# Kernel tuning notes

Hardware: AMD Instinct MI355X
Metric: run time of the kernel (lower is better)

## Reference

```python
import jax, jax.numpy as jnp
import numpy as np

B, T, I, H, R, O = 128, 512, 64, 512, 4, 64
NOISE_STD = 0.05
TAU = 0.2


def setup_inputs() -> dict:
    key = jax.random.key(0)
    ks = jax.random.split(key, 16)
    s = 0.08  # xavier-ish scale to keep gates in sane range
    return {
        "u": jax.random.normal(ks[0], (B, T, I), jnp.float32),
        "x0": jnp.zeros((B, H), jnp.float32),
        "noise": jax.random.normal(ks[1], (T, B, H), jnp.float32),
        "W_ir": jax.random.normal(ks[2], (H, I), jnp.float32) * s,
        "b_ir": jax.random.normal(ks[3], (H,), jnp.float32) * s,
        "W_iz": jax.random.normal(ks[4], (H, I), jnp.float32) * s,
        "b_iz": jax.random.normal(ks[5], (H,), jnp.float32) * s,
        "W_ih": jax.random.normal(ks[6], (H, I), jnp.float32) * s,
        "b_ih": jax.random.normal(ks[7], (H,), jnp.float32) * s,
        "N_hr": jax.random.normal(ks[8], (H, R), jnp.float32) * s,
        "M_hr": jax.random.normal(ks[9], (H, R), jnp.float32) * s,
        "N_hz": jax.random.normal(ks[10], (H, R), jnp.float32) * s,
        "M_hz": jax.random.normal(ks[11], (H, R), jnp.float32) * s,
        "N_hh": jax.random.normal(ks[12], (H, R), jnp.float32) * s,
        "M_hh": jax.random.normal(ks[13], (H, R), jnp.float32) * s,
        "W_out": jax.random.normal(ks[14], (O, H), jnp.float32) * s,
        "b_out": jax.random.normal(ks[15], (O,), jnp.float32) * s,
    }


def reference(u, x0, noise, W_ir, b_ir, W_iz, b_iz, W_ih, b_ih,
              N_hr, M_hr, N_hz, M_hz, N_hh, M_hh, W_out, b_out):
    scale = 1.0 / u.shape[-1] * 0 + 1.0 / N_hr.shape[0]  # 1/H (cont mode)
    scale = 1.0 / N_hr.shape[0]
    u_t = jnp.transpose(u, (1, 0, 2))  # [T,B,I]
    # precompute input projections for all steps (same math as per-step Linear)
    ir = jnp.einsum('tbi,hi->tbh', u_t, W_ir) + b_ir
    iz = jnp.einsum('tbi,hi->tbh', u_t, W_iz) + b_iz
    ih = jnp.einsum('tbi,hi->tbh', u_t, W_ih) + b_ih

    def step(x, inp):
        ir_t, iz_t, ih_t, n_t = inp
        hr = (x @ N_hr) @ M_hr.T * scale
        hz = (x @ N_hz) @ M_hz.T * scale
        r = jax.nn.sigmoid(ir_t + hr)
        z = jax.nn.sigmoid(iz_t + hz)
        hh = ((r * x) @ N_hh) @ M_hh.T * scale
        g = jnp.tanh(ih_t + hh)
        rec_x = (1.0 - z) * g + z * x
        x_new = x + NOISE_STD * n_t + TAU * (-x + rec_x)  # cont mode
        return x_new, x_new

    x_last, traj = jax.lax.scan(step, x0, (ir, iz, ih, noise))  # traj: [T,B,H]
    traj = jnp.transpose(traj, (1, 0, 2))  # [B,T,H]
    output = jnp.einsum('bth,oh->bto', traj, W_out) + b_out
    return output, x_last, traj
```

## Files before the change

kernel.cpp:

```cpp
#include <hip/hip_runtime.h>
#include <hip/hip_bf16.h>
#include <stdint.h>

#define Bv 128
#define Tv 512
#define Iv 64
#define Hv 512
#define Ov 64

typedef __attribute__((ext_vector_type(8))) short bv8;
typedef __attribute__((ext_vector_type(4))) float fv4;
typedef __attribute__((ext_vector_type(4))) unsigned uv4;
typedef __attribute__((ext_vector_type(2))) unsigned uv2;
typedef __attribute__((ext_vector_type(8))) unsigned short usv8;

static __device__ __forceinline__ unsigned short f2bf(float f) {
  unsigned u = __builtin_bit_cast(unsigned, f);
  u += 0x7fffu + ((u >> 16) & 1u);
  return (unsigned short)(u >> 16);
}
static __device__ __forceinline__ float bf2f(unsigned short s) {
  return __builtin_bit_cast(float, ((unsigned)s) << 16);
}
static __device__ __forceinline__ float sgm(float a) {
  return __builtin_amdgcn_rcpf(1.0f + __expf(-a));
}

template <int CTRL>
static __device__ __forceinline__ float dpp_add(float v) {
  int t = __builtin_amdgcn_update_dpp(0, __builtin_bit_cast(int, v), CTRL, 0xF, 0xF, true);
  return v + __builtin_bit_cast(float, t);
}

static __device__ __forceinline__ float wave_red(float v) {
  v = dpp_add<0xB1>(v);
  v = dpp_add<0x4E>(v);
  v = dpp_add<0x124>(v);
  v = dpp_add<0x128>(v);
  unsigned a = __builtin_bit_cast(unsigned, v);
  uv2 p = __builtin_amdgcn_permlane16_swap(a, a, false, false);
  v = __builtin_bit_cast(float, p[0]) + __builtin_bit_cast(float, p[1]);
  a = __builtin_bit_cast(unsigned, v);
  uv2 q = __builtin_amdgcn_permlane32_swap(a, a, false, false);
  v = __builtin_bit_cast(float, q[0]) + __builtin_bit_cast(float, q[1]);
  return v;
}

__global__ __launch_bounds__(256) void proj_kernel(
    const float* __restrict__ u,
    const float* __restrict__ Wir, const float* __restrict__ bir,
    const float* __restrict__ Wiz, const float* __restrict__ biz,
    const float* __restrict__ Wih, const float* __restrict__ bih,
    unsigned* __restrict__ irz, unsigned short* __restrict__ ihb)
{
  __shared__ __align__(16) unsigned short As[64][72];
  const int bt0 = blockIdx.x * 64;
  const int h0b = blockIdx.y * 64;
  const int tid = threadIdx.x;
  {
    const int r = tid >> 2, ksg = (tid & 3) * 16;
    const float* src = u + (size_t)(bt0 + r) * Iv + ksg;
    unsigned short tmp[16];
#pragma unroll
    for (int i = 0; i < 16; i += 4) {
      float4 v = *(const float4*)(src + i);
      tmp[i] = f2bf(v.x); tmp[i+1] = f2bf(v.y); tmp[i+2] = f2bf(v.z); tmp[i+3] = f2bf(v.w);
    }
    *(uv4*)&As[r][ksg]     = *(uv4*)&tmp[0];
    *(uv4*)&As[r][ksg + 8] = *(uv4*)&tmp[8];
  }
  __syncthreads();
  const int wave = tid >> 6, lane = tid & 63;
  const int n = lane & 15, q = lane >> 4;
  const int h = h0b + wave * 16 + n;
  const float* Wg[3] = {Wir, Wiz, Wih};
  bv8 bfrag[3][2];
#pragma unroll
  for (int g = 0; g < 3; ++g)
#pragma unroll
    for (int ks = 0; ks < 2; ++ks) {
      const float* wp = Wg[g] + (size_t)h * Iv + ks * 32 + q * 8;
      float4 w0 = *(const float4*)wp, w1 = *(const float4*)(wp + 4);
      bv8 f;
      f[0] = (short)f2bf(w0.x); f[1] = (short)f2bf(w0.y);
      f[2] = (short)f2bf(w0.z); f[3] = (short)f2bf(w0.w);
      f[4] = (short)f2bf(w1.x); f[5] = (short)f2bf(w1.y);
      f[6] = (short)f2bf(w1.z); f[7] = (short)f2bf(w1.w);
      bfrag[g][ks] = f;
    }
  const float bs0 = bir[h], bs1 = biz[h], bs2 = bih[h];
#pragma unroll
  for (int sub = 0; sub < 4; ++sub) {
    bv8 a0 = *(const bv8*)&As[sub * 16 + n][q * 8];
    bv8 a1 = *(const bv8*)&As[sub * 16 + n][32 + q * 8];
    fv4 ar = {0.f,0.f,0.f,0.f}, az = {0.f,0.f,0.f,0.f}, ah = {0.f,0.f,0.f,0.f};
    ar = __builtin_amdgcn_mfma_f32_16x16x32_bf16(a0, bfrag[0][0], ar, 0, 0, 0);
    ar = __builtin_amdgcn_mfma_f32_16x16x32_bf16(a1, bfrag[0][1], ar, 0, 0, 0);
    az = __builtin_amdgcn_mfma_f32_16x16x32_bf16(a0, bfrag[1][0], az, 0, 0, 0);
    az = __builtin_amdgcn_mfma_f32_16x16x32_bf16(a1, bfrag[1][1], az, 0, 0, 0);
    ah = __builtin_amdgcn_mfma_f32_16x16x32_bf16(a0, bfrag[2][0], ah, 0, 0, 0);
    ah = __builtin_amdgcn_mfma_f32_16x16x32_bf16(a1, bfrag[2][1], ah, 0, 0, 0);
#pragma unroll
    for (int j = 0; j < 4; ++j) {
      const int row = bt0 + sub * 16 + q * 4 + j;
      const size_t slot = (size_t)row * Hv + h;
      irz[slot] = ((unsigned)f2bf(az[j] + bs1) << 16) | (unsigned)f2bf(ar[j] + bs0);
      ihb[slot] = f2bf(ah[j] + bs2);
    }
  }
}

struct Buf { uv4 irz0, irz1; usv8 ih; fv4 nz0, nz1; };
#define IRZ(bf, j) ((j) < 4 ? (bf).irz0[(j)] : (bf).irz1[(j) - 4])
#define NZE(bf, j) ((j) < 4 ? (bf).nz0[(j)]  : (bf).nz1[(j) - 4])

__global__ __launch_bounds__(64, 1) void scan_kernel(
    const float* __restrict__ x0, const float* __restrict__ noise,
    const float* __restrict__ Nhr, const float* __restrict__ Mhr,
    const float* __restrict__ Nhz, const float* __restrict__ Mhz,
    const float* __restrict__ Nhh, const float* __restrict__ Mhh,
    unsigned* __restrict__ traj, const unsigned short* __restrict__ ihb,
    float* __restrict__ xlast)
{
  const int b = blockIdx.x, lane = threadIdx.x;
  const int h0 = lane * 8;
  fv4 nr[8], nz_[8], nh[8], mr[8], mz[8], mh[8];
#pragma unroll
  for (int j = 0; j < 8; ++j) {
    nr[j]  = *(const fv4*)(Nhr + (size_t)(h0 + j) * 4);
    nz_[j] = *(const fv4*)(Nhz + (size_t)(h0 + j) * 4);
    nh[j]  = *(const fv4*)(Nhh + (size_t)(h0 + j) * 4);
    mr[j]  = *(const fv4*)(Mhr + (size_t)(h0 + j) * 4);
    mz[j]  = *(const fv4*)(Mhz + (size_t)(h0 + j) * 4);
    mh[j]  = *(const fv4*)(Mhh + (size_t)(h0 + j) * 4);
  }
#pragma unroll
  for (int j = 0; j < 8; ++j) {
    asm("" : "+v"(nr[j]), "+v"(nz_[j]), "+v"(nh[j]));
    asm("" : "+v"(mr[j]), "+v"(mz[j]), "+v"(mh[j]));
  }
  float x[8];
  {
    fv4 a = *(const fv4*)(x0 + (size_t)b * Hv + h0);
    fv4 c = *(const fv4*)(x0 + (size_t)b * Hv + h0 + 4);
#pragma unroll
    for (int j = 0; j < 4; ++j) { x[j] = a[j]; x[j + 4] = c[j]; }
  }
  const size_t rowbase = (size_t)b * Tv * Hv + h0;
  const size_t nbase = (size_t)b * Hv + h0;
  Buf A, Bb;
  auto LOAD = [&](Buf& bf, int t) {
    const unsigned* p = traj + rowbase + (size_t)t * Hv;
    bf.irz0 = *(const uv4*)p;
    bf.irz1 = *(const uv4*)(p + 4);
    bf.ih = *(const usv8*)(ihb + rowbase + (size_t)t * Hv);
    const float* np = noise + (size_t)t * (Bv * Hv) + nbase;
    bf.nz0 = *(const fv4*)np;
    bf.nz1 = *(const fv4*)(np + 4);
  };
  const float sc = 1.0f / 512.0f;
  auto STEP = [&](const Buf& bf, int t) {
    float sr[4] = {0, 0, 0, 0}, sz[4] = {0, 0, 0, 0};
#pragma unroll
    for (int j = 0; j < 8; ++j)
#pragma unroll
      for (int r = 0; r < 4; ++r) {
        sr[r] = fmaf(x[j], nr[j][r], sr[r]);
        sz[r] = fmaf(x[j], nz_[j][r], sz[r]);
      }
#pragma unroll
    for (int r = 0; r < 4; ++r) {
      sr[r] = wave_red(sr[r]) * sc;
      sz[r] = wave_red(sz[r]) * sc;
    }
    float rr[8], zz[8];
#pragma unroll
    for (int j = 0; j < 8; ++j) {
      float hr = fmaf(sr[3], mr[j][3], fmaf(sr[2], mr[j][2], fmaf(sr[1], mr[j][1], sr[0] * mr[j][0])));
      float hz = fmaf(sz[3], mz[j][3], fmaf(sz[2], mz[j][2], fmaf(sz[1], mz[j][1], sz[0] * mz[j][0])));
      unsigned w = IRZ(bf, j);
      rr[j] = sgm(bf2f((unsigned short)(w & 0xffffu)) + hr);
      zz[j] = sgm(bf2f((unsigned short)(w >> 16)) + hz);
    }
    float sh[4] = {0, 0, 0, 0};
#pragma unroll
    for (int j = 0; j < 8; ++j) {
      float rx = rr[j] * x[j];
#pragma unroll
      for (int r = 0; r < 4; ++r) sh[r] = fmaf(rx, nh[j][r], sh[r]);
    }
#pragma unroll
    for (int r = 0; r < 4; ++r) sh[r] = wave_red(sh[r]) * sc;
#pragma unroll
    for (int j = 0; j < 8; ++j) {
      float hh = fmaf(sh[3], mh[j][3], fmaf(sh[2], mh[j][2], fmaf(sh[1], mh[j][1], sh[0] * mh[j][0])));
      float a = bf2f(bf.ih[j]) + hh;
      a = fminf(fmaxf(a, -15.f), 15.f);
      float e = __expf(-2.f * a);
      float g = (1.f - e) * __builtin_amdgcn_rcpf(1.f + e);
      x[j] = x[j] + 0.05f * NZE(bf, j) + 0.2f * (1.f - zz[j]) * (g - x[j]);
    }
    float* op = (float*)(traj + rowbase + (size_t)t * Hv);
    fv4 s0 = {x[0], x[1], x[2], x[3]}, s1 = {x[4], x[5], x[6], x[7]};
    *(fv4*)op = s0;
    *(fv4*)(op + 4) = s1;
  };
  LOAD(A, 0);
  for (int t = 0; t < Tv; t += 2) {
    LOAD(Bb, t + 1);
    STEP(A, t);
    if (t + 2 < Tv) LOAD(A, t + 2);
    STEP(Bb, t + 1);
  }
  {
    fv4 s0 = {x[0], x[1], x[2], x[3]}, s1 = {x[4], x[5], x[6], x[7]};
    *(fv4*)(xlast + nbase) = s0;
    *(fv4*)(xlast + nbase + 4) = s1;
  }
}

__global__ __launch_bounds__(256) void outproj_kernel(
    const float* __restrict__ traj, const float* __restrict__ Wout,
    const float* __restrict__ bout, float* __restrict__ out)
{
  __shared__ __align__(16) unsigned short As[64][40];
  const int bt0 = blockIdx.x * 64;
  const int tid = threadIdx.x;
  const int wave = tid >> 6, lane = tid & 63;
  const int n = lane & 15, q = lane >> 4;
  const int o = wave * 16 + n;
  const float bo = bout[o];
  fv4 acc[4] = {{0.f,0.f,0.f,0.f},{0.f,0.f,0.f,0.f},{0.f,0.f,0.f,0.f},{0.f,0.f,0.f,0.f}};
  const int r = tid >> 2, ksg = (tid & 3) * 8;
  for (int ks = 0; ks < 16; ++ks) {
    __syncthreads();
    {
      const float* src = traj + (size_t)(bt0 + r) * Hv + ks * 32 + ksg;
      float4 v0 = *(const float4*)src, v1 = *(const float4*)(src + 4);
      unsigned short tmp[8];
      tmp[0] = f2bf(v0.x); tmp[1] = f2bf(v0.y); tmp[2] = f2bf(v0.z); tmp[3] = f2bf(v0.w);
      tmp[4] = f2bf(v1.x); tmp[5] = f2bf(v1.y); tmp[6] = f2bf(v1.z); tmp[7] = f2bf(v1.w);
      *(uv4*)&As[r][ksg] = *(uv4*)&tmp[0];
    }
    __syncthreads();
    const float* wp = Wout + (size_t)o * Hv + ks * 32 + q * 8;
    float4 w0 = *(const float4*)wp, w1 = *(const float4*)(wp + 4);
    bv8 bf;
    bf[0] = (short)f2bf(w0.x); bf[1] = (short)f2bf(w0.y);
    bf[2] = (short)f2bf(w0.z); bf[3] = (short)f2bf(w0.w);
    bf[4] = (short)f2bf(w1.x); bf[5] = (short)f2bf(w1.y);
    bf[6] = (short)f2bf(w1.z); bf[7] = (short)f2bf(w1.w);
#pragma unroll
    for (int sub = 0; sub < 4; ++sub) {
      bv8 af = *(const bv8*)&As[sub * 16 + n][q * 8];
      acc[sub] = __builtin_amdgcn_mfma_f32_16x16x32_bf16(af, bf, acc[sub], 0, 0, 0);
    }
  }
#pragma unroll
  for (int sub = 0; sub < 4; ++sub)
#pragma unroll
    for (int j = 0; j < 4; ++j) {
      const int row = bt0 + sub * 16 + q * 4 + j;
      out[(size_t)row * Ov + o] = acc[sub][j] + bo;
    }
}

extern "C" void kernel_launch(void* const* d_in, const int* in_sizes, int n_in,
                              void* d_out, int out_size, void* d_ws, size_t ws_size,
                              hipStream_t stream) {
  const float* u    = (const float*)d_in[0];
  const float* x0   = (const float*)d_in[1];
  const float* noise= (const float*)d_in[2];
  const float* Wir  = (const float*)d_in[3];
  const float* bir  = (const float*)d_in[4];
  const float* Wiz  = (const float*)d_in[5];
  const float* biz  = (const float*)d_in[6];
  const float* Wih  = (const float*)d_in[7];
  const float* bih  = (const float*)d_in[8];
  const float* Nhr  = (const float*)d_in[9];
  const float* Mhr  = (const float*)d_in[10];
  const float* Nhz  = (const float*)d_in[11];
  const float* Mhz  = (const float*)d_in[12];
  const float* Nhh  = (const float*)d_in[13];
  const float* Mhh  = (const float*)d_in[14];
  const float* Wout = (const float*)d_in[15];
  const float* bout = (const float*)d_in[16];

  float* out   = (float*)d_out;
  float* xlast = out + (size_t)Bv * Tv * Ov;
  float* traj  = xlast + (size_t)Bv * Hv;
  unsigned short* ihbuf = (unsigned short*)d_ws;

  proj_kernel<<<dim3(1024, 8, 1), 256, 0, stream>>>(
      u, Wir, bir, Wiz, biz, Wih, bih, (unsigned*)traj, ihbuf);
  scan_kernel<<<dim3(128, 1, 1), 64, 0, stream>>>(
      x0, noise, Nhr, Mhr, Nhz, Mhz, Nhh, Mhh, (unsigned*)traj, ihbuf, xlast);
  outproj_kernel<<<dim3(1024, 1, 1), 256, 0, stream>>>(traj, Wout, bout, out);
}
```

Before: 762.4 us.

## Split each batch row's hidden dim across two waves with LDS partial-sum exchange

The scan kernel now assigns each batch element to two waves, each owning 256 hidden units at 4 per lane, and packs 4 batch elements into a 512-thread block instead of one wave per block. The two rank-4 reductions per step are combined across the wave pair through shared memory behind block-wide __syncthreads, and the 1/H scale is folded into the M matrices at load time. The aim is to halve the serial per-lane work and the size of each per-step load on the latency-bound recurrence. In exchange it adds two block barriers per timestep that also tie together the four unrelated batch elements in the block.

Result: slower. 915.7 us (+20.1%).

```diff
diff --git a/kernel.cpp b/kernel.cpp
--- a/kernel.cpp
+++ b/kernel.cpp
@@ -12,7 +12,7 @@
 typedef __attribute__((ext_vector_type(4))) float fv4;
 typedef __attribute__((ext_vector_type(4))) unsigned uv4;
 typedef __attribute__((ext_vector_type(2))) unsigned uv2;
-typedef __attribute__((ext_vector_type(8))) unsigned short usv8;
+typedef __attribute__((ext_vector_type(4))) unsigned short usv4;
 
 static __device__ __forceinline__ unsigned short f2bf(float f) {
   unsigned u = __builtin_bit_cast(unsigned, f);
@@ -110,11 +110,9 @@
   }
 }
 
-struct Buf { uv4 irz0, irz1; usv8 ih; fv4 nz0, nz1; };
-#define IRZ(bf, j) ((j) < 4 ? (bf).irz0[(j)] : (bf).irz1[(j) - 4])
-#define NZE(bf, j) ((j) < 4 ? (bf).nz0[(j)]  : (bf).nz1[(j) - 4])
-
-__global__ __launch_bounds__(64, 1) void scan_kernel(
+struct Buf { uv4 irz; usv4 ih; fv4 nz; };
+
+__global__ __launch_bounds__(512, 2) void scan_kernel(
     const float* __restrict__ x0, const float* __restrict__ noise,
     const float* __restrict__ Nhr, const float* __restrict__ Mhr,
     const float* __restrict__ Nhz, const float* __restrict__ Mhz,
@@ -122,88 +120,105 @@
     unsigned* __restrict__ traj, const unsigned short* __restrict__ ihb,
     float* __restrict__ xlast)
 {
-  const int b = blockIdx.x, lane = threadIdx.x;
-  const int h0 = lane * 8;
-  fv4 nr[8], nz_[8], nh[8], mr[8], mz[8], mh[8];
-#pragma unroll
-  for (int j = 0; j < 8; ++j) {
+  const int tid = threadIdx.x;
+  const int wave = tid >> 6, lane = tid & 63;
+  const int p = wave >> 1, half = wave & 1;
+  const int b = blockIdx.x * 4 + p;
+  const int h0 = half * 256 + lane * 4;
+  __shared__ float X1[4][2][8];
+  __shared__ float X2[4][2][4];
+
+  const float sc = 1.0f / 512.0f;
+  fv4 nr[4], nz_[4], nh[4], mr[4], mz[4], mh[4];
+#pragma unroll
+  for (int j = 0; j < 4; ++j) {
     nr[j]  = *(const fv4*)(Nhr + (size_t)(h0 + j) * 4);
     nz_[j] = *(const fv4*)(Nhz + (size_t)(h0 + j) * 4);
     nh[j]  = *(const fv4*)(Nhh + (size_t)(h0 + j) * 4);
-    mr[j]  = *(const fv4*)(Mhr + (size_t)(h0 + j) * 4);
-    mz[j]  = *(const fv4*)(Mhz + (size_t)(h0 + j) * 4);
-    mh[j]  = *(const fv4*)(Mhh + (size_t)(h0 + j) * 4);
-  }
-#pragma unroll
-  for (int j = 0; j < 8; ++j) {
+    mr[j]  = *(const fv4*)(Mhr + (size_t)(h0 + j) * 4) * sc;
+    mz[j]  = *(const fv4*)(Mhz + (size_t)(h0 + j) * 4) * sc;
+    mh[j]  = *(const fv4*)(Mhh + (size_t)(h0 + j) * 4) * sc;
+  }
+#pragma unroll
+  for (int j = 0; j < 4; ++j) {
     asm("" : "+v"(nr[j]), "+v"(nz_[j]), "+v"(nh[j]));
     asm("" : "+v"(mr[j]), "+v"(mz[j]), "+v"(mh[j]));
   }
-  float x[8];
+  float x[4];
   {
     fv4 a = *(const fv4*)(x0 + (size_t)b * Hv + h0);
-    fv4 c = *(const fv4*)(x0 + (size_t)b * Hv + h0 + 4);
-#pragma unroll
-    for (int j = 0; j < 4; ++j) { x[j] = a[j]; x[j + 4] = c[j]; }
+#pragma unroll
+    for (int j = 0; j < 4; ++j) x[j] = a[j];
   }
   const size_t rowbase = (size_t)b * Tv * Hv + h0;
   const size_t nbase = (size_t)b * Hv + h0;
   Buf A, Bb;
   auto LOAD = [&](Buf& bf, int t) {
-    const unsigned* p = traj + rowbase + (size_t)t * Hv;
-    bf.irz0 = *(const uv4*)p;
-    bf.irz1 = *(const uv4*)(p + 4);
-    bf.ih = *(const usv8*)(ihb + rowbase + (size_t)t * Hv);
-    const float* np = noise + (size_t)t * (Bv * Hv) + nbase;
-    bf.nz0 = *(const fv4*)np;
-    bf.nz1 = *(const fv4*)(np + 4);
+    bf.irz = *(const uv4*)(traj + rowbase + (size_t)t * Hv);
+    bf.ih  = *(const usv4*)(ihb + rowbase + (size_t)t * Hv);
+    bf.nz  = *(const fv4*)(noise + (size_t)t * (Bv * Hv) + nbase);
   };
-  const float sc = 1.0f / 512.0f;
   auto STEP = [&](const Buf& bf, int t) {
     float sr[4] = {0, 0, 0, 0}, sz[4] = {0, 0, 0, 0};
 #pragma unroll
-    for (int j = 0; j < 8; ++j)
+    for (int j = 0; j < 4; ++j)
 #pragma unroll
       for (int r = 0; r < 4; ++r) {
         sr[r] = fmaf(x[j], nr[j][r], sr[r]);
         sz[r] = fmaf(x[j], nz_[j][r], sz[r]);
       }
 #pragma unroll
-    for (int r = 0; r < 4; ++r) {
-      sr[r] = wave_red(sr[r]) * sc;
-      sz[r] = wave_red(sz[r]) * sc;
-    }
-    float rr[8], zz[8];
-#pragma unroll
-    for (int j = 0; j < 8; ++j) {
+    for (int r = 0; r < 4; ++r) { sr[r] = wave_red(sr[r]); sz[r] = wave_red(sz[r]); }
+    if (lane == 0) {
+      fv4 a = {sr[0], sr[1], sr[2], sr[3]}, c = {sz[0], sz[1], sz[2], sz[3]};
+      *(fv4*)&X1[p][half][0] = a;
+      *(fv4*)&X1[p][half][4] = c;
+    }
+    __syncthreads();
+    {
+      const float* o = &X1[p][half ^ 1][0];
+#pragma unroll
+      for (int r = 0; r < 4; ++r) { sr[r] += o[r]; sz[r] += o[4 + r]; }
+    }
+    float rr[4], zz[4];
+#pragma unroll
+    for (int j = 0; j < 4; ++j) {
       float hr = fmaf(sr[3], mr[j][3], fmaf(sr[2], mr[j][2], fmaf(sr[1], mr[j][1], sr[0] * mr[j][0])));
       float hz = fmaf(sz[3], mz[j][3], fmaf(sz[2], mz[j][2], fmaf(sz[1], mz[j][1], sz[0] * mz[j][0])));
-      unsigned w = IRZ(bf, j);
+      unsigned w = bf.irz[j];
       rr[j] = sgm(bf2f((unsigned short)(w & 0xffffu)) + hr);
       zz[j] = sgm(bf2f((unsigned short)(w >> 16)) + hz);
     }
     float sh[4] = {0, 0, 0, 0};
 #pragma unroll
-    for (int j = 0; j < 8; ++j) {
+    for (int j = 0; j < 4; ++j) {
       float rx = rr[j] * x[j];
 #pragma unroll
       for (int r = 0; r < 4; ++r) sh[r] = fmaf(rx, nh[j][r], sh[r]);
     }
 #pragma unroll
-    for (int r = 0; r < 4; ++r) sh[r] = wave_red(sh[r]) * sc;
-#pragma unroll
-    for (int j = 0; j < 8; ++j) {
+    for (int r = 0; r < 4; ++r) sh[r] = wave_red(sh[r]);
+    if (lane == 0) {
+      fv4 a = {sh[0], sh[1], sh[2], sh[3]};
+      *(fv4*)&X2[p][half][0] = a;
+    }
+    __syncthreads();
+    {
+      const float* o = &X2[p][half ^ 1][0];
+#pragma unroll
+      for (int r = 0; r < 4; ++r) sh[r] += o[r];
+    }
+#pragma unroll
+    for (int j = 0; j < 4; ++j) {
       float hh = fmaf(sh[3], mh[j][3], fmaf(sh[2], mh[j][2], fmaf(sh[1], mh[j][1], sh[0] * mh[j][0])));
       float a = bf2f(bf.ih[j]) + hh;
       a = fminf(fmaxf(a, -15.f), 15.f);
       float e = __expf(-2.f * a);
       float g = (1.f - e) * __builtin_amdgcn_rcpf(1.f + e);
-      x[j] = x[j] + 0.05f * NZE(bf, j) + 0.2f * (1.f - zz[j]) * (g - x[j]);
-    }
-    float* op = (float*)(traj + rowbase + (size_t)t * Hv);
-    fv4 s0 = {x[0], x[1], x[2], x[3]}, s1 = {x[4], x[5], x[6], x[7]};
-    *(fv4*)op = s0;
-    *(fv4*)(op + 4) = s1;
+      x[j] = x[j] + 0.05f * bf.nz[j] + 0.2f * (1.f - zz[j]) * (g - x[j]);
+    }
+    fv4 s0 = {x[0], x[1], x[2], x[3]};
+    *(fv4*)(traj + rowbase + (size_t)t * Hv) = s0;
   };
   LOAD(A, 0);
   for (int t = 0; t < Tv; t += 2) {
@@ -213,9 +228,8 @@
     STEP(Bb, t + 1);
   }
   {
-    fv4 s0 = {x[0], x[1], x[2], x[3]}, s1 = {x[4], x[5], x[6], x[7]};
+    fv4 s0 = {x[0], x[1], x[2], x[3]};
     *(fv4*)(xlast + nbase) = s0;
-    *(fv4*)(xlast + nbase + 4) = s1;
   }
 }
 
@@ -293,7 +307,7 @@
 
   proj_kernel<<<dim3(1024, 8, 1), 256, 0, stream>>>(
       u, Wir, bir, Wiz, biz, Wih, bih, (unsigned*)traj, ihbuf);
-  scan_kernel<<<dim3(128, 1, 1), 64, 0, stream>>>(
+  scan_kernel<<<dim3(32, 1, 1), 512, 0, stream>>>(
       x0, noise, Nhr, Mhr, Nhz, Mhz, Nhh, Mhh, (unsigned*)traj, ihbuf, xlast);
   outproj_kernel<<<dim3(1024, 1, 1), 256, 0, stream>>>(traj, Wout, bout, out);
 }
```

## Process two batch rows per scan wavefront to interleave independent recurrences

Applied to the files above, without the earlier changes.

The scan kernel now has each 64-lane wavefront advance two batch rows at once, so grid size halves from 128 to 64 blocks. The two independent chains are interleaved so their FMAs and cross-lane reductions can hide each other's latency in this latency-bound serial loop. The tanh input clamp also drops its upper bound and keeps only the lower one. The cost is half as many waves across the GPU and higher register pressure from doubled state and prefetch buffers.

Result: slower. 1.520 ms (+99.4%).

```diff
diff --git a/kernel.cpp b/kernel.cpp
--- a/kernel.cpp
+++ b/kernel.cpp
@@ -122,7 +122,7 @@
     unsigned* __restrict__ traj, const unsigned short* __restrict__ ihb,
     float* __restrict__ xlast)
 {
-  const int b = blockIdx.x, lane = threadIdx.x;
+  const int lane = threadIdx.x;
   const int h0 = lane * 8;
   fv4 nr[8], nz_[8], nh[8], mr[8], mz[8], mh[8];
 #pragma unroll
@@ -139,83 +139,104 @@
     asm("" : "+v"(nr[j]), "+v"(nz_[j]), "+v"(nh[j]));
     asm("" : "+v"(mr[j]), "+v"(mz[j]), "+v"(mh[j]));
   }
-  float x[8];
-  {
+  float x[2][8];
+  size_t rowbase[2], nbase[2];
+#pragma unroll
+  for (int g = 0; g < 2; ++g) {
+    const int b = blockIdx.x * 2 + g;
     fv4 a = *(const fv4*)(x0 + (size_t)b * Hv + h0);
     fv4 c = *(const fv4*)(x0 + (size_t)b * Hv + h0 + 4);
 #pragma unroll
-    for (int j = 0; j < 4; ++j) { x[j] = a[j]; x[j + 4] = c[j]; }
-  }
-  const size_t rowbase = (size_t)b * Tv * Hv + h0;
-  const size_t nbase = (size_t)b * Hv + h0;
-  Buf A, Bb;
-  auto LOAD = [&](Buf& bf, int t) {
-    const unsigned* p = traj + rowbase + (size_t)t * Hv;
-    bf.irz0 = *(const uv4*)p;
-    bf.irz1 = *(const uv4*)(p + 4);
-    bf.ih = *(const usv8*)(ihb + rowbase + (size_t)t * Hv);
-    const float* np = noise + (size_t)t * (Bv * Hv) + nbase;
-    bf.nz0 = *(const fv4*)np;
-    bf.nz1 = *(const fv4*)(np + 4);
+    for (int j = 0; j < 4; ++j) { x[g][j] = a[j]; x[g][j + 4] = c[j]; }
+    rowbase[g] = (size_t)b * Tv * Hv + h0;
+    nbase[g]   = (size_t)b * Hv + h0;
+  }
+  Buf PA[2], PB[2];
+  auto LOAD = [&](Buf (&bf)[2], int t) {
+#pragma unroll
+    for (int g = 0; g < 2; ++g) {
+      const unsigned* p = traj + rowbase[g] + (size_t)t * Hv;
+      bf[g].irz0 = *(const uv4*)p;
+      bf[g].irz1 = *(const uv4*)(p + 4);
+      bf[g].ih   = *(const usv8*)(ihb + rowbase[g] + (size_t)t * Hv);
+      const float* np = noise + (size_t)t * (Bv * Hv) + nbase[g];
+      bf[g].nz0 = *(const fv4*)np;
+      bf[g].nz1 = *(const fv4*)(np + 4);
+    }
   };
   const float sc = 1.0f / 512.0f;
-  auto STEP = [&](const Buf& bf, int t) {
-    float sr[4] = {0, 0, 0, 0}, sz[4] = {0, 0, 0, 0};
+  auto STEP = [&](const Buf (&bf)[2], int t) {
+    float sr[2][4] = {{0,0,0,0},{0,0,0,0}}, sz[2][4] = {{0,0,0,0},{0,0,0,0}};
 #pragma unroll
     for (int j = 0; j < 8; ++j)
 #pragma unroll
+      for (int g = 0; g < 2; ++g)
+#pragma unroll
+        for (int r = 0; r < 4; ++r) {
+          sr[g][r] = fmaf(x[g][j], nr[j][r], sr[g][r]);
+          sz[g][r] = fmaf(x[g][j], nz_[j][r], sz[g][r]);
+        }
+#pragma unroll
+    for (int g = 0; g < 2; ++g)
+#pragma unroll
       for (int r = 0; r < 4; ++r) {
-        sr[r] = fmaf(x[j], nr[j][r], sr[r]);
-        sz[r] = fmaf(x[j], nz_[j][r], sz[r]);
+        sr[g][r] = wave_red(sr[g][r]) * sc;
+        sz[g][r] = wave_red(sz[g][r]) * sc;
       }
-#pragma unroll
-    for (int r = 0; r < 4; ++r) {
-      sr[r] = wave_red(sr[r]) * sc;
-      sz[r] = wave_red(sz[r]) * sc;
-    }
-    float rr[8], zz[8];
-#pragma unroll
-    for (int j = 0; j < 8; ++j) {
-      float hr = fmaf(sr[3], mr[j][3], fmaf(sr[2], mr[j][2], fmaf(sr[1], mr[j][1], sr[0] * mr[j][0])));
-      float hz = fmaf(sz[3], mz[j][3], fmaf(sz[2], mz[j][2], fmaf(sz[1], mz[j][1], sz[0] * mz[j][0])));
-      unsigned w = IRZ(bf, j);
-      rr[j] = sgm(bf2f((unsigned short)(w & 0xffffu)) + hr);
-      zz[j] = sgm(bf2f((unsigned short)(w >> 16)) + hz);
-    }
-    float sh[4] = {0, 0, 0, 0};
-#pragma unroll
-    for (int j = 0; j < 8; ++j) {
-      float rx = rr[j] * x[j];
-#pragma unroll
-      for (int r = 0; r < 4; ++r) sh[r] = fmaf(rx, nh[j][r], sh[r]);
-    }
-#pragma unroll
-    for (int r = 0; r < 4; ++r) sh[r] = wave_red(sh[r]) * sc;
-#pragma unroll
-    for (int j = 0; j < 8; ++j) {
-      float hh = fmaf(sh[3], mh[j][3], fmaf(sh[2], mh[j][2], fmaf(sh[1], mh[j][1], sh[0] * mh[j][0])));
-      float a = bf2f(bf.ih[j]) + hh;
-      a = fminf(fmaxf(a, -15.f), 15.f);
-      float e = __expf(-2.f * a);
-      float g = (1.f - e) * __builtin_amdgcn_rcpf(1.f + e);
-      x[j] = x[j] + 0.05f * NZE(bf, j) + 0.2f * (1.f - zz[j]) * (g - x[j]);
-    }
-    float* op = (float*)(traj + rowbase + (size_t)t * Hv);
-    fv4 s0 = {x[0], x[1], x[2], x[3]}, s1 = {x[4], x[5], x[6], x[7]};
-    *(fv4*)op = s0;
-    *(fv4*)(op + 4) = s1;
+    float rx[2][8], zz[2][8];
+#pragma unroll
+    for (int j = 0; j < 8; ++j)
+#pragma unroll
+      for (int g = 0; g < 2; ++g) {
+        float hr = fmaf(sr[g][3], mr[j][3], fmaf(sr[g][2], mr[j][2], fmaf(sr[g][1], mr[j][1], sr[g][0] * mr[j][0])));
+        float hz = fmaf(sz[g][3], mz[j][3], fmaf(sz[g][2], mz[j][2], fmaf(sz[g][1], mz[j][1], sz[g][0] * mz[j][0])));
+        unsigned w = IRZ(bf[g], j);
+        rx[g][j] = sgm(bf2f((unsigned short)(w & 0xffffu)) + hr) * x[g][j];
+        zz[g][j] = sgm(bf2f((unsigned short)(w >> 16)) + hz);
+      }
+    float sh[2][4] = {{0,0,0,0},{0,0,0,0}};
+#pragma unroll
+    for (int j = 0; j < 8; ++j)
+#pragma unroll
+      for (int g = 0; g < 2; ++g)
+#pragma unroll
+        for (int r = 0; r < 4; ++r) sh[g][r] = fmaf(rx[g][j], nh[j][r], sh[g][r]);
+#pragma unroll
+    for (int g = 0; g < 2; ++g)
+#pragma unroll
+      for (int r = 0; r < 4; ++r) sh[g][r] = wave_red(sh[g][r]) * sc;
+#pragma unroll
+    for (int j = 0; j < 8; ++j)
+#pragma unroll
+      for (int g = 0; g < 2; ++g) {
+        float hh = fmaf(sh[g][3], mh[j][3], fmaf(sh[g][2], mh[j][2], fmaf(sh[g][1], mh[j][1], sh[g][0] * mh[j][0])));
+        float a = fmaxf(bf2f(bf[g].ih[j]) + hh, -15.f);
+        float e = __expf(-2.f * a);
+        float g_ = (1.f - e) * __builtin_amdgcn_rcpf(1.f + e);
+        x[g][j] = x[g][j] + 0.05f * NZE(bf[g], j) + 0.2f * (1.f - zz[g][j]) * (g_ - x[g][j]);
+      }
+#pragma unroll
+    for (int g = 0; g < 2; ++g) {
+      float* op = (float*)(traj + rowbase[g] + (size_t)t * Hv);
+      fv4 s0 = {x[g][0], x[g][1], x[g][2], x[g][3]};
+      fv4 s1 = {x[g][4], x[g][5], x[g][6], x[g][7]};
+      *(fv4*)op = s0;
+      *(fv4*)(op + 4) = s1;
+    }
   };
-  LOAD(A, 0);
+  LOAD(PA, 0);
   for (int t = 0; t < Tv; t += 2) {
-    LOAD(Bb, t + 1);
-    STEP(A, t);
-    if (t + 2 < Tv) LOAD(A, t + 2);
-    STEP(Bb, t + 1);
-  }
-  {
-    fv4 s0 = {x[0], x[1], x[2], x[3]}, s1 = {x[4], x[5], x[6], x[7]};
-    *(fv4*)(xlast + nbase) = s0;
-    *(fv4*)(xlast + nbase + 4) = s1;
+    LOAD(PB, t + 1);
+    STEP(PA, t);
+    if (t + 2 < Tv) LOAD(PA, t + 2);
+    STEP(PB, t + 1);
+  }
+#pragma unroll
+  for (int g = 0; g < 2; ++g) {
+    fv4 s0 = {x[g][0], x[g][1], x[g][2], x[g][3]};
+    fv4 s1 = {x[g][4], x[g][5], x[g][6], x[g][7]};
+    *(fv4*)(xlast + nbase[g]) = s0;
+    *(fv4*)(xlast + nbase[g] + 4) = s1;
   }
 }
 
@@ -293,7 +314,7 @@
 
   proj_kernel<<<dim3(1024, 8, 1), 256, 0, stream>>>(
       u, Wir, bir, Wiz, biz, Wih, bih, (unsigned*)traj, ihbuf);
-  scan_kernel<<<dim3(128, 1, 1), 64, 0, stream>>>(
+  scan_kernel<<<dim3(64, 1, 1), 64, 0, stream>>>(
       x0, noise, Nhr, Mhr, Nhz, Mhz, Nhh, Mhh, (unsigned*)traj, ihbuf, xlast);
   outproj_kernel<<<dim3(1024, 1, 1), 256, 0, stream>>>(traj, Wout, bout, out);
 }
```
